# Optimization experiments

Hardware: AMD Instinct MI355X
Metric: run time of the kernel (lower is better)

Reference implementation:

```python
import jax, jax.numpy as jnp
import numpy as np

N_BITS = 14
L = 1 << N_BITS
B, C_IN, C_OUT = 32, 32, 64

def _neigh_idx():
    # (L, n_bits): index j flipped at bit b -> j ^ (1<<b)
    s = jnp.arange(L)
    return jnp.stack([s ^ (1 << b) for b in range(N_BITS)], axis=1)

def setup_inputs() -> dict:
    key = jax.random.key(0)
    k1, k2, k3, k4 = jax.random.split(key, 4)
    x = jax.random.normal(k1, (B, C_IN, L), dtype=jnp.float32)
    w_self = jnp.ones((), dtype=jnp.float32)
    w_bits = jax.random.normal(k2, (N_BITS,), dtype=jnp.float32) * 0.1
    # Conv1d(kernel_size=1) weight squeezed to (C_out, C_in)
    mix_w = jax.random.normal(k3, (C_OUT, C_IN), dtype=jnp.float32) * (1.0 / np.sqrt(C_IN))
    mix_b = jax.random.normal(k4, (C_OUT,), dtype=jnp.float32) * 0.01
    return {"x": x, "w_self": w_self, "w_bits": w_bits, "mix_w": mix_w, "mix_b": mix_b}

def reference(x, w_self, w_bits, mix_w, mix_b):
    n_bits = w_bits.shape[0]
    idx = _neigh_idx()                          # (L, n_bits), int32
    xn = x[:, :, idx]                           # (B, C, L, n_bits) XOR-neighbor gather
    neigh_sum = jnp.einsum('bclk,k->bcl', xn, w_bits)
    y = w_self * x + neigh_sum
    y = y / (1.0 + n_bits)                      # agg == 'mean'
    # 1x1 conv mix: (B,C,L) x (C_out,C_in) -> (B,C_out,L)
    return jnp.einsum('bcl,oc->bol', y, mix_w) + mix_b[None, :, None]
```

## Files before the change

### kernel.cpp

```cpp
#include <hip/hip_runtime.h>

#define TILE  256
#define CIN   32
#define COUT  64
#define LSIZE 16384
#define NBITS 14

__global__ __launch_bounds__(256, 4)
void hamming_fused(const float* __restrict__ x,
                   const float* __restrict__ w_self,
                   const float* __restrict__ w_bits,
                   const float* __restrict__ mix_w,
                   const float* __restrict__ mix_b,
                   float* __restrict__ out)
{
    __shared__ float xs[CIN][TILE];
    __shared__ float mws[CIN][COUT];

    const int tid  = threadIdx.x;
    const int tile = blockIdx.x;
    const int b    = blockIdx.y;
    const int base = tile * TILE;
    const float* xb = x + (size_t)b * CIN * LSIZE;

    #pragma unroll
    for (int i = 0; i < (CIN * COUT) / 256; ++i) {
        int g = tid + i * 256;
        int o = g >> 5, c = g & 31;
        mws[c][o] = mix_w[g];
    }

    #pragma unroll
    for (int i = 0; i < (CIN * TILE) / (256 * 4); ++i) {
        int idx = tid + i * 256;
        int r  = idx >> 6;
        int c4 = (idx & 63) << 2;
        *(float4*)&xs[r][c4] =
            *(const float4*)(xb + (size_t)r * LSIZE + base + c4);
    }
    __syncthreads();

    const float ws = w_self[0];
    float wb[NBITS];
    #pragma unroll
    for (int k = 0; k < NBITS; ++k) wb[k] = w_bits[k];

    const int t    = tid;
    const int gcol = base + t;
    float yreg[CIN];

    #pragma unroll 4
    for (int c = 0; c < CIN; ++c) {
        const float* xr = xb + (size_t)c * LSIZE;
        float a = ws * xs[c][t];
        #pragma unroll
        for (int k = 0; k < 8; ++k)
            a += wb[k] * xs[c][t ^ (1 << k)];
        #pragma unroll
        for (int k = 8; k < NBITS; ++k)
            a += wb[k] * xr[gcol ^ (1 << k)];
        yreg[c] = a * (1.0f / 15.0f);
    }
    __syncthreads();

    #pragma unroll
    for (int c = 0; c < CIN; ++c) xs[c][t] = yreg[c];
    __syncthreads();

    const int tx   = tid & 63;
    const int ty   = tid >> 6;
    const int colb = tx << 2;
    const int o0   = ty * 16;

    float4 acc[16];
    #pragma unroll
    for (int j = 0; j < 16; ++j) {
        float bias = mix_b[o0 + j];
        acc[j] = make_float4(bias, bias, bias, bias);
    }

    #pragma unroll 4
    for (int c = 0; c < CIN; ++c) {
        float4 yv = *(float4*)&xs[c][colb];
        #pragma unroll
        for (int j4 = 0; j4 < 4; ++j4) {
            float4 m = *(float4*)&mws[c][o0 + j4 * 4];
            acc[j4*4+0].x += m.x * yv.x; acc[j4*4+0].y += m.x * yv.y;
            acc[j4*4+0].z += m.x * yv.z; acc[j4*4+0].w += m.x * yv.w;
            acc[j4*4+1].x += m.y * yv.x; acc[j4*4+1].y += m.y * yv.y;
            acc[j4*4+1].z += m.y * yv.z; acc[j4*4+1].w += m.y * yv.w;
            acc[j4*4+2].x += m.z * yv.x; acc[j4*4+2].y += m.z * yv.y;
            acc[j4*4+2].z += m.z * yv.z; acc[j4*4+2].w += m.z * yv.w;
            acc[j4*4+3].x += m.w * yv.x; acc[j4*4+3].y += m.w * yv.y;
            acc[j4*4+3].z += m.w * yv.z; acc[j4*4+3].w += m.w * yv.w;
        }
    }

    float* ob = out + (size_t)b * COUT * LSIZE;
    #pragma unroll
    for (int j = 0; j < 16; ++j) {
        *(float4*)(ob + (size_t)(o0 + j) * LSIZE + base + colb) = acc[j];
    }
}

extern "C" void kernel_launch(void* const* d_in, const int* in_sizes, int n_in,
                              void* d_out, int out_size, void* d_ws, size_t ws_size,
                              hipStream_t stream) {
    const float* x      = (const float*)d_in[0];
    const float* w_self = (const float*)d_in[1];
    const float* w_bits = (const float*)d_in[2];
    const float* mix_w  = (const float*)d_in[3];
    const float* mix_b  = (const float*)d_in[4];
    float* out = (float*)d_out;

    dim3 grid(LSIZE / TILE, 32);
    hamming_fused<<<grid, 256, 0, stream>>>(x, w_self, w_bits, mix_w, mix_b, out);
}
```

Baseline: 225.2 us.

## Remap blocks per XCD, batch far-neighbor loads, use nontemporal output stores

```diff
diff --git a/kernel.cpp b/kernel.cpp
--- a/kernel.cpp
+++ b/kernel.cpp
@@ -5,6 +5,8 @@
 #define COUT  64
 #define LSIZE 16384
 #define NBITS 14
+
+typedef float vfloat4 __attribute__((ext_vector_type(4)));
 
 __global__ __launch_bounds__(256, 4)
 void hamming_fused(const float* __restrict__ x,
@@ -17,9 +19,13 @@
     __shared__ float xs[CIN][TILE];
     __shared__ float mws[CIN][COUT];
 
-    const int tid  = threadIdx.x;
-    const int tile = blockIdx.x;
-    const int b    = blockIdx.y;
+    const int tid = threadIdx.x;
+
+    const int d    = blockIdx.x;
+    const int xcd  = d & 7;
+    const int j    = d >> 3;
+    const int b    = xcd * 4 + (j >> 6);
+    const int tile = j & 63;
     const int base = tile * TILE;
     const float* xb = x + (size_t)b * CIN * LSIZE;
 
@@ -49,17 +55,28 @@
     const int gcol = base + t;
     float yreg[CIN];
 
-    #pragma unroll 4
-    for (int c = 0; c < CIN; ++c) {
-        const float* xr = xb + (size_t)c * LSIZE;
-        float a = ws * xs[c][t];
+    #pragma unroll
+    for (int c0 = 0; c0 < CIN; c0 += 8) {
+        float pf[8][6];
         #pragma unroll
-        for (int k = 0; k < 8; ++k)
-            a += wb[k] * xs[c][t ^ (1 << k)];
+        for (int cc = 0; cc < 8; ++cc) {
+            const float* xr = xb + (size_t)(c0 + cc) * LSIZE;
+            #pragma unroll
+            for (int k = 0; k < 6; ++k)
+                pf[cc][k] = xr[gcol ^ (TILE << k)];
+        }
         #pragma unroll
-        for (int k = 8; k < NBITS; ++k)
-            a += wb[k] * xr[gcol ^ (1 << k)];
-        yreg[c] = a * (1.0f / 15.0f);
+        for (int cc = 0; cc < 8; ++cc) {
+            int c = c0 + cc;
+            float a = ws * xs[c][t];
+            #pragma unroll
+            for (int k = 0; k < 8; ++k)
+                a += wb[k] * xs[c][t ^ (1 << k)];
+            #pragma unroll
+            for (int k = 0; k < 6; ++k)
+                a += wb[8 + k] * pf[cc][k];
+            yreg[c] = a * (1.0f / 15.0f);
+        }
     }
     __syncthreads();
 
@@ -74,9 +91,9 @@
 
     float4 acc[16];
     #pragma unroll
-    for (int j = 0; j < 16; ++j) {
-        float bias = mix_b[o0 + j];
-        acc[j] = make_float4(bias, bias, bias, bias);
+    for (int jj = 0; jj < 16; ++jj) {
+        float bias = mix_b[o0 + jj];
+        acc[jj] = make_float4(bias, bias, bias, bias);
     }
 
     #pragma unroll 4
@@ -98,8 +115,10 @@
 
     float* ob = out + (size_t)b * COUT * LSIZE;
     #pragma unroll
-    for (int j = 0; j < 16; ++j) {
-        *(float4*)(ob + (size_t)(o0 + j) * LSIZE + base + colb) = acc[j];
+    for (int jj = 0; jj < 16; ++jj) {
+        vfloat4 v; v.x = acc[jj].x; v.y = acc[jj].y; v.z = acc[jj].z; v.w = acc[jj].w;
+        vfloat4* p = (vfloat4*)(ob + (size_t)(o0 + jj) * LSIZE + base + colb);
+        __builtin_nontemporal_store(v, p);
     }
 }
 
@@ -113,6 +132,5 @@
     const float* mix_b  = (const float*)d_in[4];
     float* out = (float*)d_out;
 
-    dim3 grid(LSIZE / TILE, 32);
-    hamming_fused<<<grid, 256, 0, stream>>>(x, w_self, w_bits, mix_w, mix_b, out);
+    hamming_fused<<<dim3(2048), 256, 0, stream>>>(x, w_self, w_bits, mix_w, mix_b, out);
 }
```

Result: faster. 210.5 us (-6.5%).
